# Kernel optimization log

Measured on AMD Instinct MI355X. Metric: run time of the kernel, lower is better.

Reference implementation:

```python
import jax, jax.numpy as jnp
import numpy as np

STATE_DIM = 256
ACT_LEN = 16
LATENT = 256
ENC = 512
SLOPE = 0.01  # torch.nn.LeakyReLU() default


def _leaky(x):
    return jnp.where(x >= 0, x, SLOPE * x)


def setup_inputs() -> dict:
    key = jax.random.key(0)
    ks = jax.random.split(key, 16)
    B, T = 64, 1024
    D = STATE_DIM + 2 * ACT_LEN
    s = lambda k, shp, fan_in: jax.random.normal(k, shp, dtype=jnp.float32) * (1.0 / np.sqrt(fan_in))
    return {
        "padded_input": jax.random.normal(ks[0], (B, T, D), dtype=jnp.float32),
        # encoder: Linear(state,enc)+leaky, Linear(enc,enc)+leaky, Linear(enc,latent)+leaky
        "enc_w1": s(ks[1], (STATE_DIM, ENC), STATE_DIM), "enc_b1": jnp.zeros((ENC,), jnp.float32),
        "enc_w2": s(ks[2], (ENC, ENC), ENC),             "enc_b2": jnp.zeros((ENC,), jnp.float32),
        "enc_w3": s(ks[3], (ENC, LATENT), ENC),          "enc_b3": jnp.zeros((LATENT,), jnp.float32),
        # latent dynamics (bias-free)
        "A_w": s(ks[4], (LATENT, LATENT), LATENT),
        "B_w": s(ks[5], (ACT_LEN, LATENT), ACT_LEN),
        # decoder: Linear(latent,enc)+leaky, Linear(enc,enc)+leaky, Linear(enc,state)
        "dec_w1": s(ks[6], (LATENT, ENC), LATENT),       "dec_b1": jnp.zeros((ENC,), jnp.float32),
        "dec_w2": s(ks[7], (ENC, ENC), ENC),             "dec_b2": jnp.zeros((ENC,), jnp.float32),
        "dec_w3": s(ks[8], (ENC, STATE_DIM), ENC),       "dec_b3": jnp.zeros((STATE_DIM,), jnp.float32),
    }


def reference(padded_input, enc_w1, enc_b1, enc_w2, enc_b2, enc_w3, enc_b3,
              A_w, B_w, dec_w1, dec_b1, dec_w2, dec_b2, dec_w3, dec_b3):
    # slice features: [state | u_t | u_t1]
    x_t = padded_input[:, :, :STATE_DIM]                       # [B,T,S]
    u_t1 = padded_input[:, :, STATE_DIM + ACT_LEN:]            # [B,T,A]

    # encoder MLP
    h = _leaky(x_t @ enc_w1 + enc_b1)
    h = _leaky(h @ enc_w2 + enc_b2)
    z_t = _leaky(h @ enc_w3 + enc_b3)                          # [B,T,L]

    # reset_probability=0, nwarmup=0: t=0 uses z_t[:,0], then pure recurrence
    # z1[t] = A z1[t-1] + B u_t1[t]
    Bu = u_t1 @ B_w                                            # [B,T,L]

    def step(prev, bu_t):
        new = prev @ A_w + bu_t                                # [B,L]
        return new, new

    _, z1 = jax.lax.scan(step, z_t[:, 0, :], jnp.swapaxes(Bu, 0, 1))
    z_t1 = jnp.swapaxes(z1, 0, 1)                              # [B,T,L]

    # decoder MLP (last layer linear)
    h = _leaky(z_t1 @ dec_w1 + dec_b1)
    h = _leaky(h @ dec_w2 + dec_b2)
    x_t1 = h @ dec_w3 + dec_b3                                 # [B,T,S]
    return x_t1
```

## Files before the change

### kernel.cpp

```cpp
#include <hip/hip_runtime.h>

constexpr int Bb  = 64;
constexpr int Tt  = 1024;
constexpr int Dd  = 288;
constexpr int Ss  = 256;
constexpr int ALa = 16;
constexpr int Ll  = 256;
constexpr int Ee  = 512;
constexpr int CC  = 8;
constexpr int NCh = 128;
constexpr int NSC = 16;
constexpr int SC  = 8;
constexpr int DEC_CHUNKS = 8;
constexpr int DEC_ROWS = (Bb*Tt)/DEC_CHUNKS;

#define LKY(v) ((v) >= 0.f ? (v) : 0.01f*(v))

using f32x4  = __attribute__((ext_vector_type(4))) float;
using short8 = __attribute__((ext_vector_type(8))) short;
typedef unsigned short ushort_t;

__device__ __forceinline__ unsigned short f2bf(float f){
  unsigned int u = __float_as_uint(f);
  u = (u + 0x7fffu + ((u >> 16) & 1u)) >> 16;
  return (unsigned short)u;
}
__device__ __forceinline__ float bf2f(unsigned short h){
  return __uint_as_float(((unsigned int)h) << 16);
}

__global__ __launch_bounds__(256) void enc_dense(
    const float* __restrict__ xin, int xstride,
    const float* __restrict__ W, const float* __restrict__ bias,
    float* __restrict__ out, int K, int N, int act)
{
  int b = blockIdx.x, col0 = blockIdx.y * 32;
  int tid = threadIdx.x;
  int tx = tid & 31, tk = tid >> 5;
  __shared__ float x[512];
  __shared__ float part[8][33];
  for (int k = tid; k < K; k += 256) x[k] = xin[(long)b*xstride + k];
  __syncthreads();
  int j = col0 + tx;
  float p0=0.f,p1=0.f,p2=0.f,p3=0.f;
  int iters = K >> 3;
  #pragma unroll 2
  for (int i = 0; i < iters; i += 4){
    int k0 = tk + 8*i;
    p0 = fmaf(x[k0     ], W[(long)(k0     )*N + j], p0);
    p1 = fmaf(x[k0 +  8], W[(long)(k0 +  8)*N + j], p1);
    p2 = fmaf(x[k0 + 16], W[(long)(k0 + 16)*N + j], p2);
    p3 = fmaf(x[k0 + 24], W[(long)(k0 + 24)*N + j], p3);
  }
  part[tk][tx] = (p0+p1)+(p2+p3);
  __syncthreads();
  if (tid < 32){
    float s = part[0][tid];
    #pragma unroll
    for (int q = 1; q < 8; ++q) s += part[q][tid];
    s += bias[col0 + tid];
    out[b*N + col0 + tid] = act ? LKY(s) : s;
  }
}

__global__ __launch_bounds__(256) void matmul_g(
    const float* __restrict__ X, const float* __restrict__ Y,
    float* __restrict__ Cf, ushort_t* __restrict__ Ch, ushort_t* __restrict__ Cl)
{
  int i = blockIdx.x;
  int tid = threadIdx.x;
  int jg = tid & 63, tk = tid >> 6;
  __shared__ float row[256];
  __shared__ float4 part[4][64];
  if (tid < 256) row[tid] = X[i*256 + tid];
  __syncthreads();
  int j4 = jg*4;
  float4 p0 = make_float4(0,0,0,0), p1 = make_float4(0,0,0,0);
  int kb = tk*64;
  #pragma unroll 4
  for (int k = kb; k < kb+64; k += 2){
    float x0 = row[k], x1 = row[k+1];
    float4 y0 = *(const float4*)&Y[(k  )*256 + j4];
    float4 y1 = *(const float4*)&Y[(k+1)*256 + j4];
    p0.x = fmaf(x0,y0.x,p0.x); p0.y = fmaf(x0,y0.y,p0.y);
    p0.z = fmaf(x0,y0.z,p0.z); p0.w = fmaf(x0,y0.w,p0.w);
    p1.x = fmaf(x1,y1.x,p1.x); p1.y = fmaf(x1,y1.y,p1.y);
    p1.z = fmaf(x1,y1.z,p1.z); p1.w = fmaf(x1,y1.w,p1.w);
  }
  p0.x+=p1.x; p0.y+=p1.y; p0.z+=p1.z; p0.w+=p1.w;
  part[tk][jg] = p0;
  __syncthreads();
  if (tid < 64){
    float4 s = part[0][tid];
    #pragma unroll
    for (int q = 1; q < 4; ++q){
      float4 v = part[q][tid];
      s.x+=v.x; s.y+=v.y; s.z+=v.z; s.w+=v.w;
    }
    int j = tid*4;
    if (Cf) *(float4*)&Cf[i*256 + j] = s;
    if (Ch){
      float vv[4] = {s.x,s.y,s.z,s.w};
      #pragma unroll
      for (int e = 0; e < 4; ++e){
        ushort_t h = f2bf(vv[e]);
        int o = ((i>>3)*256 + j + e)*8 + (i&7);
        Ch[o] = h; Cl[o] = f2bf(vv[e] - bf2f(h));
      }
    }
  }
}

__global__ __launch_bounds__(256) void prep_w(
    const float* __restrict__ W, ushort_t* __restrict__ Wh,
    ushort_t* __restrict__ Wl, int N)
{
  int o = blockIdx.x*256 + threadIdx.x;
  int j = o & 7;
  int rest = o >> 3;
  int n = rest % N;
  int t8 = rest / N;
  int k = t8*8 + j;
  float v = W[k*N + n];
  ushort_t h = f2bf(v);
  Wh[o] = h;
  Wl[o] = f2bf(v - bf2f(h));
}

__global__ __launch_bounds__(256) void prep_bw(
    const float* __restrict__ B, ushort_t* __restrict__ Bh, ushort_t* __restrict__ Bl)
{
  int o = blockIdx.x*256 + threadIdx.x;
  int j = o & 7, rest = o >> 3;
  int n = rest & 255, kq = rest >> 8;
  int k = kq*8 + j;
  float v = (k < ALa) ? B[k*256 + n] : 0.f;
  ushort_t h = f2bf(v);
  Bh[o] = h; Bl[o] = f2bf(v - bf2f(h));
}

__device__ __forceinline__ void load_afrag(
    const ushort_t* __restrict__ P, int kq, int m0, short8* dst)
{
  #pragma unroll
  for (int mt = 0; mt < 4; ++mt)
    dst[mt] = *(const short8*)&P[((long)kq*256 + m0 + mt*16)*8];
}

__global__ __launch_bounds__(256) void scan_mfma(
    const float* __restrict__ in0,
    const ushort_t* __restrict__ AtH, const ushort_t* __restrict__ AtL,
    const ushort_t* __restrict__ BtH, const ushort_t* __restrict__ BtL,
    float* __restrict__ wend, float* __restrict__ zout)
{
  int chunk = blockIdx.x;
  int tid = threadIdx.x;
  int wave = tid >> 6, lane = tid & 63;
  int quad = lane >> 4, l16 = lane & 15;
  int mwave = wave * 64;
  int m0 = mwave + l16;

  __shared__ ushort_t StH[16384];
  __shared__ ushort_t StL[16384];

  short8 Bfh[4], Bfl[4];
  #pragma unroll
  for (int mt = 0; mt < 4; ++mt){
    int off = ((quad)*256 + m0 + mt*16)*8;
    Bfh[mt] = *(const short8*)&BtH[off];
    Bfl[mt] = *(const short8*)&BtL[off];
  }

  f32x4 acc[4][4];
  #pragma unroll
  for (int mt = 0; mt < 4; ++mt)
    #pragma unroll
    for (int nt = 0; nt < 4; ++nt) acc[mt][nt] = (f32x4){0.f,0.f,0.f,0.f};

  const float* ubase[4];
  #pragma unroll
  for (int nt = 0; nt < 4; ++nt)
    ubase[nt] = in0 + (long)(nt*16 + l16)*(Tt*Dd) + (Ss + ALa) + quad*8;

  short8 Ahb[2][4], Alb[2][4];

  for (int tt = 0; tt < CC; ++tt){
    int t = chunk*CC + tt;
    float4 uq[4][2];
    #pragma unroll
    for (int nt = 0; nt < 4; ++nt){
      if (quad < 2){
        const float* up = ubase[nt] + (long)t*Dd;
        uq[nt][0] = *(const float4*)up;
        uq[nt][1] = *(const float4*)(up + 4);
      } else {
        uq[nt][0] = make_float4(0,0,0,0); uq[nt][1] = make_float4(0,0,0,0);
      }
    }

    if (tt > 0){
      load_afrag(AtH, 0*4 + quad, m0, Ahb[0]);
      load_afrag(AtL, 0*4 + quad, m0, Alb[0]);
      #pragma unroll
      for (int kt = 0; kt < 8; ++kt){
        int cur = kt & 1;
        if (kt < 7){
          load_afrag(AtH, (kt+1)*4 + quad, m0, Ahb[cur^1]);
          load_afrag(AtL, (kt+1)*4 + quad, m0, Alb[cur^1]);
        }
        short8 Sbh[4], Sbl[4];
        #pragma unroll
        for (int nt = 0; nt < 4; ++nt){
          int off = ((kt*4 + quad)*64 + nt*16 + l16)*8;
          Sbh[nt] = *(const short8*)&StH[off];
          Sbl[nt] = *(const short8*)&StL[off];
        }
        #pragma unroll
        for (int mt = 0; mt < 4; ++mt)
          #pragma unroll
          for (int nt = 0; nt < 4; ++nt){
            acc[mt][nt] = __builtin_amdgcn_mfma_f32_16x16x32_bf16(Ahb[cur][mt], Sbh[nt], acc[mt][nt], 0,0,0);
            acc[mt][nt] = __builtin_amdgcn_mfma_f32_16x16x32_bf16(Ahb[cur][mt], Sbl[nt], acc[mt][nt], 0,0,0);
            acc[mt][nt] = __builtin_amdgcn_mfma_f32_16x16x32_bf16(Alb[cur][mt], Sbh[nt], acc[mt][nt], 0,0,0);
          }
      }
    }

    short8 uh[4], ul[4];
    #pragma unroll
    for (int nt = 0; nt < 4; ++nt){
      float v[8] = {uq[nt][0].x,uq[nt][0].y,uq[nt][0].z,uq[nt][0].w,
                    uq[nt][1].x,uq[nt][1].y,uq[nt][1].z,uq[nt][1].w};
      ushort_t hs[8], ls[8];
      #pragma unroll
      for (int j = 0; j < 8; ++j){
        hs[j] = f2bf(v[j]);
        ls[j] = f2bf(v[j] - bf2f(hs[j]));
      }
      uh[nt] = *(const short8*)hs; ul[nt] = *(const short8*)ls;
    }
    #pragma unroll
    for (int mt = 0; mt < 4; ++mt)
      #pragma unroll
      for (int nt = 0; nt < 4; ++nt){
        acc[mt][nt] = __builtin_amdgcn_mfma_f32_16x16x32_bf16(Bfh[mt], uh[nt], acc[mt][nt], 0,0,0);
        acc[mt][nt] = __builtin_amdgcn_mfma_f32_16x16x32_bf16(Bfh[mt], ul[nt], acc[mt][nt], 0,0,0);
        acc[mt][nt] = __builtin_amdgcn_mfma_f32_16x16x32_bf16(Bfl[mt], uh[nt], acc[mt][nt], 0,0,0);
      }

    __syncthreads();

    #pragma unroll
    for (int mt = 0; mt < 4; ++mt){
      int mb = mwave + mt*16 + quad*4;
      #pragma unroll
      for (int nt = 0; nt < 4; ++nt){
        int n = nt*16 + l16;
        f32x4 v = acc[mt][nt];
        *(float4*)&zout[((long)n*Tt + t)*Ll + mb] = make_float4(v[0],v[1],v[2],v[3]);
        if (tt == CC-1)
          *(float4*)&wend[((long)chunk*Bb + n)*Ll + mb] = make_float4(v[0],v[1],v[2],v[3]);
        #pragma unroll
        for (int reg = 0; reg < 4; ++reg){
          int m = mb + reg;
          ushort_t h = f2bf(v[reg]);
          ushort_t l = f2bf(v[reg] - bf2f(h));
          int so = ((m>>3)*64 + n)*8 + (m&7);
          StH[so] = h; StL[so] = l;
        }
        acc[mt][nt] = (f32x4){0.f,0.f,0.f,0.f};
      }
    }
    __syncthreads();
  }
}

__device__ __forceinline__ void frag_init_state512(
    const float* __restrict__ src, ushort_t* StH, ushort_t* StL, int tid)
{
  #pragma unroll
  for (int it = 0; it < 4; ++it){
    int idx = tid + it*512;
    int m8 = idx >> 6, n = idx & 63;
    const float* p = src + (long)n*256 + m8*8;
    float4 v0 = *(const float4*)p;
    float4 v1 = *(const float4*)(p + 4);
    float vv[8] = {v0.x,v0.y,v0.z,v0.w,v1.x,v1.y,v1.z,v1.w};
    ushort_t hs[8], ls[8];
    #pragma unroll
    for (int j = 0; j < 8; ++j){
      hs[j] = f2bf(vv[j]);
      ls[j] = f2bf(vv[j] - bf2f(hs[j]));
    }
    *(uint4*)&StH[(m8*64 + n)*8] = *(const uint4*)hs;
    *(uint4*)&StL[(m8*64 + n)*8] = *(const uint4*)ls;
  }
}

__device__ __forceinline__ void p2_load_A(
    const ushort_t* __restrict__ PH, const ushort_t* __restrict__ PL,
    int wave, int lane, short8 Ah[2][8], short8 Al[2][8])
{
  int quad = lane >> 4, l16 = lane & 15;
  int m0 = wave*32 + l16;
  #pragma unroll
  for (int kt = 0; kt < 8; ++kt){
    int kq = kt*4 + quad;
    #pragma unroll
    for (int mt = 0; mt < 2; ++mt){
      Ah[mt][kt] = *(const short8*)&PH[((long)kq*256 + m0 + mt*16)*8];
      Al[mt][kt] = *(const short8*)&PL[((long)kq*256 + m0 + mt*16)*8];
    }
  }
}

__device__ __forceinline__ void p2_step_w(
    const short8 Ah[2][8], const short8 Al[2][8],
    const float* __restrict__ addin,
    ushort_t* StH, ushort_t* StL,
    float* __restrict__ out_f32,
    int wave, int lane)
{
  int quad = lane >> 4, l16 = lane & 15;
  int mwave = wave*32;

  f32x4 acc[2][4];
  #pragma unroll
  for (int mt = 0; mt < 2; ++mt){
    int mb = mwave + mt*16 + quad*4;
    #pragma unroll
    for (int nt = 0; nt < 4; ++nt){
      int n = nt*16 + l16;
      float4 v = *(const float4*)&addin[(long)n*256 + mb];
      acc[mt][nt] = (f32x4){v.x, v.y, v.z, v.w};
    }
  }

  #pragma unroll
  for (int kt = 0; kt < 8; ++kt){
    #pragma unroll
    for (int nt = 0; nt < 4; ++nt){
      int off = ((kt*4 + quad)*64 + nt*16 + l16)*8;
      short8 Sbh = *(const short8*)&StH[off];
      short8 Sbl = *(const short8*)&StL[off];
      #pragma unroll
      for (int mt = 0; mt < 2; ++mt){
        acc[mt][nt] = __builtin_amdgcn_mfma_f32_16x16x32_bf16(Ah[mt][kt], Sbh, acc[mt][nt], 0,0,0);
        acc[mt][nt] = __builtin_amdgcn_mfma_f32_16x16x32_bf16(Ah[mt][kt], Sbl, acc[mt][nt], 0,0,0);
        acc[mt][nt] = __builtin_amdgcn_mfma_f32_16x16x32_bf16(Al[mt][kt], Sbh, acc[mt][nt], 0,0,0);
      }
    }
  }

  __syncthreads();

  #pragma unroll
  for (int mt = 0; mt < 2; ++mt){
    int mb = mwave + mt*16 + quad*4;
    #pragma unroll
    for (int nt = 0; nt < 4; ++nt){
      int n = nt*16 + l16;
      f32x4 v = acc[mt][nt];
      if (out_f32)
        *(float4*)&out_f32[(long)n*256 + mb] = make_float4(v[0],v[1],v[2],v[3]);
      #pragma unroll
      for (int reg = 0; reg < 4; ++reg){
        int m = mb + reg;
        ushort_t h = f2bf(v[reg]);
        int so = ((m>>3)*64 + n)*8 + (m&7);
        StH[so] = h;
        StL[so] = f2bf(v[reg] - bf2f(h));
      }
    }
  }
  __syncthreads();
}

__global__ __launch_bounds__(512) void pass2_local_mfma(
    const ushort_t* __restrict__ A8H, const ushort_t* __restrict__ A8L,
    const float* __restrict__ wend, float* __restrict__ lend)
{
  int s = blockIdx.x;
  int tid = threadIdx.x;
  int wave = tid >> 6, lane = tid & 63;
  __shared__ ushort_t StH[16384], StL[16384];
  short8 Ah[2][8], Al[2][8];
  p2_load_A(A8H, A8L, wave, lane, Ah, Al);
  frag_init_state512(wend + (long)(s*SC)*Bb*256, StH, StL, tid);
  __syncthreads();
  for (int i = 1; i < SC; ++i)
    p2_step_w(Ah, Al, wend + (long)(s*SC + i)*Bb*256, StH, StL,
              (i == SC-1) ? (lend + (long)s*Bb*256) : nullptr, wave, lane);
}

__global__ __launch_bounds__(512) void pass2_global_mfma(
    const ushort_t* __restrict__ A64H, const ushort_t* __restrict__ A64L,
    const float* __restrict__ lend, float* __restrict__ inits)
{
  int tid = threadIdx.x;
  int wave = tid >> 6, lane = tid & 63;
  __shared__ ushort_t StH[16384], StL[16384];
  short8 Ah[2][8], Al[2][8];
  p2_load_A(A64H, A64L, wave, lane, Ah, Al);
  frag_init_state512(inits, StH, StL, tid);
  __syncthreads();
  for (int s = 0; s < NSC-1; ++s)
    p2_step_w(Ah, Al, lend + (long)s*Bb*256, StH, StL,
              inits + (long)((s+1)*SC)*Bb*256, wave, lane);
}

__global__ __launch_bounds__(512) void pass2_replay_mfma(
    const ushort_t* __restrict__ A8H, const ushort_t* __restrict__ A8L,
    const float* __restrict__ wend, float* __restrict__ inits)
{
  int s = blockIdx.x;
  int tid = threadIdx.x;
  int wave = tid >> 6, lane = tid & 63;
  __shared__ ushort_t StH[16384], StL[16384];
  short8 Ah[2][8], Al[2][8];
  p2_load_A(A8H, A8L, wave, lane, Ah, Al);
  frag_init_state512(inits + (long)(s*SC)*Bb*256, StH, StL, tid);
  __syncthreads();
  for (int i = 0; i < SC-1; ++i)
    p2_step_w(Ah, Al, wend + (long)(s*SC + i)*Bb*256, StH, StL,
              inits + (long)(s*SC + i + 1)*Bb*256, wave, lane);
}

__global__ __launch_bounds__(256) void gemm_corr(
    const float* __restrict__ inits, const ushort_t* __restrict__ AjH,
    const ushort_t* __restrict__ AjL, float* __restrict__ out)
{
  int jz = blockIdx.z;
  const ushort_t* Whp = AjH + (long)jz*65536;
  const ushort_t* Wlp = AjL + (long)jz*65536;
  __shared__ __align__(16) ushort_t Xh[4*128*8], Xl[4*128*8];
  __shared__ __align__(16) ushort_t Wh[4*128*8], Wl[4*128*8];

  int tid  = threadIdx.x;
  int wave = tid >> 6, lane = tid & 63;
  int wm = wave & 1, wn = wave >> 1;
  int quad = lane >> 4, l16 = lane & 15;
  int row0 = blockIdx.y * 128;
  int col0 = blockIdx.x * 128;

  f32x4 acc[4][4];
  #pragma unroll
  for (int mt = 0; mt < 4; ++mt)
    #pragma unroll
    for (int nt = 0; nt < 4; ++nt) acc[mt][nt] = (f32x4){0.f,0.f,0.f,0.f};

  for (int kt = 0; kt < 8; ++kt){
    #pragma unroll
    for (int it = 0; it < 2; ++it){
      int idx = tid + it*256;
      int q = idx >> 7, m = idx & 127;
      const float* xp = &inits[(long)(row0 + m)*256 + kt*32 + q*8];
      float4 v0 = *(const float4*)xp;
      float4 v1 = *(const float4*)(xp + 4);
      float vv[8] = {v0.x,v0.y,v0.z,v0.w,v1.x,v1.y,v1.z,v1.w};
      ushort_t hs[8], ls[8];
      #pragma unroll
      for (int j = 0; j < 8; ++j){
        hs[j] = f2bf(vv[j]);
        ls[j] = f2bf(vv[j] - bf2f(hs[j]));
      }
      *(uint4*)&Xh[(q*128 + m)*8] = *(const uint4*)hs;
      *(uint4*)&Xl[(q*128 + m)*8] = *(const uint4*)ls;
      int n = idx & 127;
      long src = (long)(kt*4 + q)*256 + col0 + n;
      ((uint4*)Wh)[q*128 + n] = ((const uint4*)Whp)[src];
      ((uint4*)Wl)[q*128 + n] = ((const uint4*)Wlp)[src];
    }
    __syncthreads();
    short8 ah[4], al[4], bh[4], bl[4];
    #pragma unroll
    for (int mt = 0; mt < 4; ++mt){
      int off = (quad*128 + wm*64 + mt*16 + l16)*8;
      ah[mt] = *(const short8*)&Xh[off];
      al[mt] = *(const short8*)&Xl[off];
    }
    #pragma unroll
    for (int nt = 0; nt < 4; ++nt){
      int off = (quad*128 + wn*64 + nt*16 + l16)*8;
      bh[nt] = *(const short8*)&Wh[off];
      bl[nt] = *(const short8*)&Wl[off];
    }
    #pragma unroll
    for (int mt = 0; mt < 4; ++mt)
      #pragma unroll
      for (int nt = 0; nt < 4; ++nt){
        acc[mt][nt] = __builtin_amdgcn_mfma_f32_16x16x32_bf16(ah[mt], bh[nt], acc[mt][nt], 0,0,0);
        acc[mt][nt] = __builtin_amdgcn_mfma_f32_16x16x32_bf16(ah[mt], bl[nt], acc[mt][nt], 0,0,0);
        acc[mt][nt] = __builtin_amdgcn_mfma_f32_16x16x32_bf16(al[mt], bh[nt], acc[mt][nt], 0,0,0);
      }
    __syncthreads();
  }

  #pragma unroll
  for (int mt = 0; mt < 4; ++mt){
    #pragma unroll
    for (int nt = 0; nt < 4; ++nt){
      int col = col0 + wn*64 + nt*16 + l16;
      #pragma unroll
      for (int reg = 0; reg < 4; ++reg){
        int row = row0 + wm*64 + mt*16 + quad*4 + reg;
        int b = row & 63, c = row >> 6;
        int t = c*CC + jz;
        long addr = ((long)b*Tt + t)*Ll + col;
        out[addr] += acc[mt][nt][reg];
      }
    }
  }
}

template<int BM, int BN, bool INS, bool OUTS>
__global__ __launch_bounds__(256) void gemm_mfma(
    const float* __restrict__ X,
    const ushort_t* __restrict__ Xhp, const ushort_t* __restrict__ Xlp,
    const ushort_t* __restrict__ Whp, const ushort_t* __restrict__ Wlp,
    const float* __restrict__ bias, float* __restrict__ Y,
    ushort_t* __restrict__ Yh, ushort_t* __restrict__ Yl,
    int Mrows, int K, int N, int act)
{
  constexpr int BMh = BM/2, BNh = BN/2;
  constexpr int MT = BM/32, NT = BN/32;
  __shared__ __align__(16) ushort_t Xh[4*BM*8], Xl[4*BM*8];
  __shared__ __align__(16) ushort_t Wh[4*BN*8], Wl[4*BN*8];

  int tid  = threadIdx.x;
  int wave = tid >> 6, lane = tid & 63;
  int wm = wave & 1, wn = wave >> 1;
  int quad = lane >> 4, l16 = lane & 15;
  long row0 = (long)blockIdx.y * BM;
  int col0 = blockIdx.x * BN;

  f32x4 acc[MT][NT];
  #pragma unroll
  for (int mt = 0; mt < MT; ++mt)
    #pragma unroll
    for (int nt = 0; nt < NT; ++nt) acc[mt][nt] = (f32x4){0.f,0.f,0.f,0.f};

  for (int kt = 0; kt < K; kt += 32){
    int ktile = kt >> 5;
    if constexpr (INS){
      #pragma unroll
      for (int it = 0; it < (BM*4)/256; ++it){
        int idx = tid + it*256;
        int q = idx / BM, m = idx % BM;
        long src = (long)(ktile*4 + q)*Mrows + row0 + m;
        ((uint4*)Xh)[q*BM + m] = ((const uint4*)Xhp)[src];
        ((uint4*)Xl)[q*BM + m] = ((const uint4*)Xlp)[src];
      }
    } else {
      #pragma unroll
      for (int it = 0; it < (BM*4)/256; ++it){
        int idx = tid + it*256;
        int q = idx / BM, m = idx % BM;
        const float* xp = &X[(row0 + m)*(long)K + kt + q*8];
        float4 v0 = *(const float4*)xp;
        float4 v1 = *(const float4*)(xp + 4);
        float vv[8] = {v0.x,v0.y,v0.z,v0.w,v1.x,v1.y,v1.z,v1.w};
        ushort_t hs[8], ls[8];
        #pragma unroll
        for (int j = 0; j < 8; ++j){
          hs[j] = f2bf(vv[j]);
          ls[j] = f2bf(vv[j] - bf2f(hs[j]));
        }
        *(uint4*)&Xh[(q*BM + m)*8] = *(const uint4*)hs;
        *(uint4*)&Xl[(q*BM + m)*8] = *(const uint4*)ls;
      }
    }
    #pragma unroll
    for (int it = 0; it < (BN*4)/256; ++it){
      int idx = tid + it*256;
      int q = idx / BN, n = idx % BN;
      long src = (long)(ktile*4 + q)*N + col0 + n;
      ((uint4*)Wh)[q*BN + n] = ((const uint4*)Whp)[src];
      ((uint4*)Wl)[q*BN + n] = ((const uint4*)Wlp)[src];
    }
    __syncthreads();

    short8 ah[MT], al[MT], bh[NT], bl[NT];
    #pragma unroll
    for (int mt = 0; mt < MT; ++mt){
      int off = (quad*BM + wm*BMh + mt*16 + l16)*8;
      ah[mt] = *(const short8*)&Xh[off];
      al[mt] = *(const short8*)&Xl[off];
    }
    #pragma unroll
    for (int nt = 0; nt < NT; ++nt){
      int off = (quad*BN + wn*BNh + nt*16 + l16)*8;
      bh[nt] = *(const short8*)&Wh[off];
      bl[nt] = *(const short8*)&Wl[off];
    }
    #pragma unroll
    for (int mt = 0; mt < MT; ++mt)
      #pragma unroll
      for (int nt = 0; nt < NT; ++nt){
        acc[mt][nt] = __builtin_amdgcn_mfma_f32_16x16x32_bf16(ah[mt], bh[nt], acc[mt][nt], 0, 0, 0);
        acc[mt][nt] = __builtin_amdgcn_mfma_f32_16x16x32_bf16(ah[mt], bl[nt], acc[mt][nt], 0, 0, 0);
        acc[mt][nt] = __builtin_amdgcn_mfma_f32_16x16x32_bf16(al[mt], bh[nt], acc[mt][nt], 0, 0, 0);
      }
    __syncthreads();
  }

  #pragma unroll
  for (int mt = 0; mt < MT; ++mt){
    long rowb = row0 + wm*BMh + mt*16 + quad*4;
    #pragma unroll
    for (int nt = 0; nt < NT; ++nt){
      int col = col0 + wn*BNh + nt*16 + l16;
      float bs = bias[col];
      #pragma unroll
      for (int reg = 0; reg < 4; ++reg){
        float y = acc[mt][nt][reg] + bs;
        if (act) y = LKY(y);
        long row = rowb + reg;
        if constexpr (OUTS){
          ushort_t h = f2bf(y);
          ushort_t l = f2bf(y - bf2f(h));
          long off = ((long)(col >> 3)*Mrows + row)*8 + (col & 7);
          Yh[off] = h; Yl[off] = l;
        } else {
          Y[row*(long)N + col] = y;
        }
      }
    }
  }
}

extern "C" void kernel_launch(void* const* d_in, const int* in_sizes, int n_in,
                              void* d_out, int out_size, void* d_ws, size_t ws_size,
                              hipStream_t stream) {
  const float* in0    = (const float*)d_in[0];
  const float* enc_w1 = (const float*)d_in[1];
  const float* enc_b1 = (const float*)d_in[2];
  const float* enc_w2 = (const float*)d_in[3];
  const float* enc_b2 = (const float*)d_in[4];
  const float* enc_w3 = (const float*)d_in[5];
  const float* enc_b3 = (const float*)d_in[6];
  const float* A_w    = (const float*)d_in[7];
  const float* B_w    = (const float*)d_in[8];
  const float* dec_w1 = (const float*)d_in[9];
  const float* dec_b1 = (const float*)d_in[10];
  const float* dec_w2 = (const float*)d_in[11];
  const float* dec_b2 = (const float*)d_in[12];
  const float* dec_w3 = (const float*)d_in[13];
  const float* dec_b3 = (const float*)d_in[14];
  float* out = (float*)d_out;

  float* ws    = (float*)d_ws;
  float* h1enc = ws;
  float* h2enc = ws + 32768;
  float* s2    = ws + 65536;
  float* s3    = ws + 131072;
  float* s4    = ws + 196608;
  float* s8    = ws + 262144;
  float* s16   = ws + 327680;
  float* s32   = ws + 393216;
  float* s64   = ws + 458752;
  ushort_t* Whp_d = (ushort_t*)(ws + 524288);
  ushort_t* Wlp_d = (ushort_t*)(ws + 786432);
  float* Rf    = ws + 1048576;
  ushort_t* AjH = (ushort_t*)Rf;
  ushort_t* AjL = (ushort_t*)(Rf + 262144);
  ushort_t* BtH = (ushort_t*)(Rf + 524288);
  ushort_t* BtL = BtH + 8192;
  float* wend  = Rf + 532480;
  float* inits = Rf + 2629632;
  float* lend  = Rf + 4726784;
  ushort_t* A64H = (ushort_t*)(Rf + 4988928);
  ushort_t* A64L = (ushort_t*)(Rf + 5021696);
  ushort_t* h1h = (ushort_t*)Rf;
  ushort_t* h1l = (ushort_t*)(Rf + 2097152);
  ushort_t* h2h = (ushort_t*)(Rf + 4194304);
  ushort_t* h2l = (ushort_t*)(Rf + 6291456);
  ushort_t* A8H = AjH + 7*65536;
  ushort_t* A8L = AjL + 7*65536;

  enc_dense<<<dim3(64,16), 256, 0, stream>>>(in0, Tt*Dd, enc_w1, enc_b1, h1enc, 256, 512, 1);
  enc_dense<<<dim3(64,16), 256, 0, stream>>>(h1enc, 512, enc_w2, enc_b2, h2enc, 512, 512, 1);
  enc_dense<<<dim3(64, 8), 256, 0, stream>>>(h2enc, 512, enc_w3, enc_b3, inits, 512, 256, 1);

  prep_w<<<256, 256, 0, stream>>>(A_w, AjH, AjL, 256);
  prep_bw<<<32, 256, 0, stream>>>(B_w, BtH, BtL);
  matmul_g<<<256, 256, 0, stream>>>(A_w, A_w, s2, AjH+1*65536, AjL+1*65536);
  matmul_g<<<256, 256, 0, stream>>>(s2, A_w, s3, AjH+2*65536, AjL+2*65536);
  matmul_g<<<256, 256, 0, stream>>>(s2, s2, s4, AjH+3*65536, AjL+3*65536);
  matmul_g<<<256, 256, 0, stream>>>(s4, A_w, nullptr, AjH+4*65536, AjL+4*65536);
  matmul_g<<<256, 256, 0, stream>>>(s4, s2, nullptr, AjH+5*65536, AjL+5*65536);
  matmul_g<<<256, 256, 0, stream>>>(s4, s3, nullptr, AjH+6*65536, AjL+6*65536);
  matmul_g<<<256, 256, 0, stream>>>(s4, s4, s8, A8H, A8L);
  matmul_g<<<256, 256, 0, stream>>>(s8, s8, s16, nullptr, nullptr);
  matmul_g<<<256, 256, 0, stream>>>(s16, s16, s32, nullptr, nullptr);
  matmul_g<<<256, 256, 0, stream>>>(s32, s32, s64, A64H, A64L);

  prep_w<<<512,  256, 0, stream>>>(dec_w1, Whp_d,          Wlp_d,          512);
  prep_w<<<1024, 256, 0, stream>>>(dec_w2, Whp_d + 131072, Wlp_d + 131072, 512);
  prep_w<<<512,  256, 0, stream>>>(dec_w3, Whp_d + 393216, Wlp_d + 393216, 256);

  scan_mfma<<<NCh, 256, 0, stream>>>(in0, AjH, AjL, BtH, BtL, wend, out);
  pass2_local_mfma <<<NSC, 512, 0, stream>>>(A8H, A8L, wend, lend);
  pass2_global_mfma<<<1,   512, 0, stream>>>(A64H, A64L, lend, inits);
  pass2_replay_mfma<<<NSC, 512, 0, stream>>>(A8H, A8L, wend, inits);
  gemm_corr<<<dim3(2, 64, 8), 256, 0, stream>>>(inits, AjH, AjL, out);

  for (int rc = 0; rc < DEC_CHUNKS; ++rc){
    const float* zc = out + (long)rc*DEC_ROWS*Ll;
    float* oc       = out + (long)rc*DEC_ROWS*Ll;
    gemm_mfma<64,128,false,true><<<dim3(Ee/128, DEC_ROWS/64), 256, 0, stream>>>(
        zc, nullptr, nullptr, Whp_d, Wlp_d, dec_b1, nullptr, h1h, h1l, DEC_ROWS, Ll, Ee, 1);
    gemm_mfma<64,128,true,true><<<dim3(Ee/128, DEC_ROWS/64), 256, 0, stream>>>(
        nullptr, h1h, h1l, Whp_d + 131072, Wlp_d + 131072, dec_b2, nullptr, h2h, h2l, DEC_ROWS, Ee, Ee, 1);
    gemm_mfma<64,128,true,false><<<dim3(Ss/128, DEC_ROWS/64), 256, 0, stream>>>(
        nullptr, h2h, h2l, Whp_d + 393216, Wlp_d + 393216, dec_b3, oc, nullptr, nullptr, DEC_ROWS, Ee, Ss, 0);
  }
}
```

Baseline: 1.007 ms.

## Replace serial pass-2 chunk recurrences with Kogge-Stone parallel prefix rounds

```diff
diff --git a/kernel.cpp b/kernel.cpp
--- a/kernel.cpp
+++ b/kernel.cpp
@@ -314,16 +314,20 @@
   }
 }
 
-__device__ __forceinline__ void p2_step_w(
-    const short8 Ah[2][8], const short8 Al[2][8],
-    const float* __restrict__ addin,
-    ushort_t* StH, ushort_t* StL,
-    float* __restrict__ out_f32,
-    int wave, int lane)
-{
+__device__ __forceinline__ void ks_gemm_body(
+    const ushort_t* __restrict__ PH, const ushort_t* __restrict__ PL,
+    const float* __restrict__ accsrc, const float* __restrict__ bsrc,
+    float* __restrict__ outp, ushort_t* StH, ushort_t* StL)
+{
+  int tid = threadIdx.x;
+  int wave = tid >> 6, lane = tid & 63;
   int quad = lane >> 4, l16 = lane & 15;
   int mwave = wave*32;
 
+  short8 Ah[2][8], Al[2][8];
+  p2_load_A(PH, PL, wave, lane, Ah, Al);
+  frag_init_state512(bsrc, StH, StL, tid);
+
   f32x4 acc[2][4];
   #pragma unroll
   for (int mt = 0; mt < 2; ++mt){
@@ -331,10 +335,11 @@
     #pragma unroll
     for (int nt = 0; nt < 4; ++nt){
       int n = nt*16 + l16;
-      float4 v = *(const float4*)&addin[(long)n*256 + mb];
+      float4 v = *(const float4*)&accsrc[(long)n*256 + mb];
       acc[mt][nt] = (f32x4){v.x, v.y, v.z, v.w};
     }
   }
+  __syncthreads();
 
   #pragma unroll
   for (int kt = 0; kt < 8; ++kt){
@@ -352,8 +357,6 @@
     }
   }
 
-  __syncthreads();
-
   #pragma unroll
   for (int mt = 0; mt < 2; ++mt){
     int mb = mwave + mt*16 + quad*4;
@@ -361,69 +364,54 @@
     for (int nt = 0; nt < 4; ++nt){
       int n = nt*16 + l16;
       f32x4 v = acc[mt][nt];
-      if (out_f32)
-        *(float4*)&out_f32[(long)n*256 + mb] = make_float4(v[0],v[1],v[2],v[3]);
-      #pragma unroll
-      for (int reg = 0; reg < 4; ++reg){
-        int m = mb + reg;
-        ushort_t h = f2bf(v[reg]);
-        int so = ((m>>3)*64 + n)*8 + (m&7);
-        StH[so] = h;
-        StL[so] = f2bf(v[reg] - bf2f(h));
-      }
-    }
-  }
-  __syncthreads();
-}
-
-__global__ __launch_bounds__(512) void pass2_local_mfma(
-    const ushort_t* __restrict__ A8H, const ushort_t* __restrict__ A8L,
-    const float* __restrict__ wend, float* __restrict__ lend)
-{
-  int s = blockIdx.x;
+      *(float4*)&outp[(long)n*256 + mb] = make_float4(v[0],v[1],v[2],v[3]);
+    }
+  }
+}
+
+__device__ __forceinline__ const float* ks_src(
+    const float* __restrict__ in, const float* __restrict__ z0,
+    const float* __restrict__ pbend, int c, int init_mode)
+{
+  if (!init_mode) return in + (long)c*(Bb*Ll);
+  return (c == 0) ? z0 : (pbend + (long)(8*c - 1)*(Bb*Ll));
+}
+
+__global__ __launch_bounds__(512) void ks_round(
+    const ushort_t* __restrict__ PH, const ushort_t* __restrict__ PL,
+    const float* __restrict__ in, const float* __restrict__ z0,
+    const float* __restrict__ pbend,
+    float* __restrict__ out, long outStride, int d, int local_seg, int init_mode)
+{
+  int c = blockIdx.x;
   int tid = threadIdx.x;
-  int wave = tid >> 6, lane = tid & 63;
+  int pos = local_seg ? (c & 7) : c;
+  const float* src_c = ks_src(in, z0, pbend, c, init_mode);
+  float* op = out + (long)c*outStride;
+
+  if (pos < d){
+    const float4* s4p = (const float4*)src_c;
+    float4* d4p = (float4*)op;
+    #pragma unroll
+    for (int it = 0; it < 8; ++it) d4p[tid + it*512] = s4p[tid + it*512];
+    return;
+  }
+  const float* src_cd = ks_src(in, z0, pbend, c - d, init_mode);
   __shared__ ushort_t StH[16384], StL[16384];
-  short8 Ah[2][8], Al[2][8];
-  p2_load_A(A8H, A8L, wave, lane, Ah, Al);
-  frag_init_state512(wend + (long)(s*SC)*Bb*256, StH, StL, tid);
-  __syncthreads();
-  for (int i = 1; i < SC; ++i)
-    p2_step_w(Ah, Al, wend + (long)(s*SC + i)*Bb*256, StH, StL,
-              (i == SC-1) ? (lend + (long)s*Bb*256) : nullptr, wave, lane);
-}
-
-__global__ __launch_bounds__(512) void pass2_global_mfma(
-    const ushort_t* __restrict__ A64H, const ushort_t* __restrict__ A64L,
-    const float* __restrict__ lend, float* __restrict__ inits)
-{
-  int tid = threadIdx.x;
-  int wave = tid >> 6, lane = tid & 63;
+  ks_gemm_body(PH, PL, src_c, src_cd, op, StH, StL);
+}
+
+__global__ __launch_bounds__(512) void replay_corr(
+    const ushort_t* __restrict__ A8PH, const ushort_t* __restrict__ A8PL,
+    const float* __restrict__ pb, float* __restrict__ inits)
+{
+  int i = blockIdx.x + 1;
+  int s = blockIdx.y;
   __shared__ ushort_t StH[16384], StL[16384];
-  short8 Ah[2][8], Al[2][8];
-  p2_load_A(A64H, A64L, wave, lane, Ah, Al);
-  frag_init_state512(inits, StH, StL, tid);
-  __syncthreads();
-  for (int s = 0; s < NSC-1; ++s)
-    p2_step_w(Ah, Al, lend + (long)s*Bb*256, StH, StL,
-              inits + (long)((s+1)*SC)*Bb*256, wave, lane);
-}
-
-__global__ __launch_bounds__(512) void pass2_replay_mfma(
-    const ushort_t* __restrict__ A8H, const ushort_t* __restrict__ A8L,
-    const float* __restrict__ wend, float* __restrict__ inits)
-{
-  int s = blockIdx.x;
-  int tid = threadIdx.x;
-  int wave = tid >> 6, lane = tid & 63;
-  __shared__ ushort_t StH[16384], StL[16384];
-  short8 Ah[2][8], Al[2][8];
-  p2_load_A(A8H, A8L, wave, lane, Ah, Al);
-  frag_init_state512(inits + (long)(s*SC)*Bb*256, StH, StL, tid);
-  __syncthreads();
-  for (int i = 0; i < SC-1; ++i)
-    p2_step_w(Ah, Al, wend + (long)(s*SC + i)*Bb*256, StH, StL,
-              inits + (long)(s*SC + i + 1)*Bb*256, wave, lane);
+  ks_gemm_body(A8PH + (long)(i-1)*65536, A8PL + (long)(i-1)*65536,
+               pb + (long)(8*s + i - 1)*(Bb*Ll),
+               inits + (long)(8*s)*(Bb*Ll),
+               inits + (long)(8*s + i)*(Bb*Ll), StH, StL);
 }
 
 __global__ __launch_bounds__(256) void gemm_corr(
@@ -668,9 +656,18 @@
   ushort_t* BtL = BtH + 8192;
   float* wend  = Rf + 532480;
   float* inits = Rf + 2629632;
-  float* lend  = Rf + 4726784;
+  float* g0    = Rf + 4726784;
   ushort_t* A64H = (ushort_t*)(Rf + 4988928);
   ushort_t* A64L = (ushort_t*)(Rf + 5021696);
+  float* pb0   = Rf + 5054464;
+  ushort_t* A8PH = (ushort_t*)(Rf + 7151616);
+  ushort_t* A8PL = (ushort_t*)(Rf + 7380992);
+  ushort_t* A64PH = (ushort_t*)(Rf + 7610368);
+  ushort_t* A64PL = (ushort_t*)(Rf + 7708672);
+  float* f24   = Rf + 7806976;
+  float* f128  = Rf + 7872512;
+  float* f256  = Rf + 7938048;
+  float* g1    = Rf + 8003584;
   ushort_t* h1h = (ushort_t*)Rf;
   ushort_t* h1l = (ushort_t*)(Rf + 2097152);
   ushort_t* h2h = (ushort_t*)(Rf + 4194304);
@@ -691,18 +688,33 @@
   matmul_g<<<256, 256, 0, stream>>>(s4, s2, nullptr, AjH+5*65536, AjL+5*65536);
   matmul_g<<<256, 256, 0, stream>>>(s4, s3, nullptr, AjH+6*65536, AjL+6*65536);
   matmul_g<<<256, 256, 0, stream>>>(s4, s4, s8, A8H, A8L);
-  matmul_g<<<256, 256, 0, stream>>>(s8, s8, s16, nullptr, nullptr);
-  matmul_g<<<256, 256, 0, stream>>>(s16, s16, s32, nullptr, nullptr);
+  prep_w<<<256, 256, 0, stream>>>(s8, A8PH, A8PL, 256);
+  matmul_g<<<256, 256, 0, stream>>>(s8, s8, s16, A8PH+1*65536, A8PL+1*65536);
+  matmul_g<<<256, 256, 0, stream>>>(s16, s8, f24, A8PH+2*65536, A8PL+2*65536);
+  matmul_g<<<256, 256, 0, stream>>>(s16, s16, s32, A8PH+3*65536, A8PL+3*65536);
+  matmul_g<<<256, 256, 0, stream>>>(s32, s8, nullptr, A8PH+4*65536, A8PL+4*65536);
+  matmul_g<<<256, 256, 0, stream>>>(s32, s16, nullptr, A8PH+5*65536, A8PL+5*65536);
+  matmul_g<<<256, 256, 0, stream>>>(s32, f24, nullptr, A8PH+6*65536, A8PL+6*65536);
   matmul_g<<<256, 256, 0, stream>>>(s32, s32, s64, A64H, A64L);
+  matmul_g<<<256, 256, 0, stream>>>(s64, s64, f128, A64PH+0*65536, A64PL+0*65536);
+  matmul_g<<<256, 256, 0, stream>>>(f128, f128, f256, A64PH+1*65536, A64PL+1*65536);
+  matmul_g<<<256, 256, 0, stream>>>(f256, f256, nullptr, A64PH+2*65536, A64PL+2*65536);
 
   prep_w<<<512,  256, 0, stream>>>(dec_w1, Whp_d,          Wlp_d,          512);
   prep_w<<<1024, 256, 0, stream>>>(dec_w2, Whp_d + 131072, Wlp_d + 131072, 512);
   prep_w<<<512,  256, 0, stream>>>(dec_w3, Whp_d + 393216, Wlp_d + 393216, 256);
 
   scan_mfma<<<NCh, 256, 0, stream>>>(in0, AjH, AjL, BtH, BtL, wend, out);
-  pass2_local_mfma <<<NSC, 512, 0, stream>>>(A8H, A8L, wend, lend);
-  pass2_global_mfma<<<1,   512, 0, stream>>>(A64H, A64L, lend, inits);
-  pass2_replay_mfma<<<NSC, 512, 0, stream>>>(A8H, A8L, wend, inits);
+
+  ks_round<<<128, 512, 0, stream>>>(A8H, A8L, wend, nullptr, nullptr, pb0, Bb*Ll, 1, 1, 0);
+  ks_round<<<128, 512, 0, stream>>>(A8PH+1*65536, A8PL+1*65536, pb0, nullptr, nullptr, wend, Bb*Ll, 2, 1, 0);
+  ks_round<<<128, 512, 0, stream>>>(A8PH+3*65536, A8PL+3*65536, wend, nullptr, nullptr, pb0, Bb*Ll, 4, 1, 0);
+  ks_round<<<16, 512, 0, stream>>>(A64H, A64L, nullptr, inits, pb0, g1, Bb*Ll, 1, 0, 1);
+  ks_round<<<16, 512, 0, stream>>>(A64PH+0*65536, A64PL+0*65536, g1, nullptr, nullptr, g0, Bb*Ll, 2, 0, 0);
+  ks_round<<<16, 512, 0, stream>>>(A64PH+1*65536, A64PL+1*65536, g0, nullptr, nullptr, g1, Bb*Ll, 4, 0, 0);
+  ks_round<<<16, 512, 0, stream>>>(A64PH+2*65536, A64PL+2*65536, g1, nullptr, nullptr, inits, (long)SC*Bb*Ll, 8, 0, 0);
+  replay_corr<<<dim3(7, 16), 512, 0, stream>>>(A8PH, A8PL, pb0, inits);
+
   gemm_corr<<<dim3(2, 64, 8), 256, 0, stream>>>(inits, AjH, AjL, out);
 
   for (int rc = 0; rc < DEC_CHUNKS; ++rc){
```

New measurement: 984.5 us. 2.2% less time.
